# Optimization experiments

Hardware: AMD Instinct MI355X
Metric: run time of the kernel (lower is better)

The kernel has to match this reference:

```python
import jax, jax.numpy as jnp
import numpy as np

N_ADAPTERS = 16
RANK = 16
ALPHA = 16.0
SCALING = ALPHA / RANK
B, S, IN, OUT = 32, 512, 1024, 4096


def setup_inputs() -> dict:
    key = jax.random.key(0)
    k1, k2, k3, k4, k5, k6 = jax.random.split(key, 6)
    hidden_states = jax.random.normal(k1, (B, S, IN), dtype=jnp.float32)
    adapter_ids = jax.random.randint(k2, (B,), 0, N_ADAPTERS, dtype=jnp.int64)
    W = jax.random.normal(k3, (IN, OUT), dtype=jnp.float32) * 0.02
    b = jax.random.normal(k4, (OUT,), dtype=jnp.float32) * 0.02
    lora_a = jax.random.normal(k5, (N_ADAPTERS, IN, RANK), dtype=jnp.float32) * (1.0 / np.sqrt(IN))
    lora_b = jax.random.normal(k6, (N_ADAPTERS, RANK, OUT), dtype=jnp.float32) * 0.02
    return {"hidden_states": hidden_states, "adapter_ids": adapter_ids,
            "W": W, "b": b, "lora_a": lora_a, "lora_b": lora_b}


def reference(hidden_states, adapter_ids, W, b, lora_a, lora_b):
    # Base Conv1D (GPT-2 style): x @ W + b  -> [B, S, OUT]
    base_output = jnp.einsum('bsi,io->bso', hidden_states, W) + b
    # Per-sample adapter gather (replaces the unique-id loop + boolean masks):
    a_sel = lora_a[adapter_ids]          # [B, IN, R]
    b_sel = lora_b[adapter_ids]          # [B, R, OUT]
    low_rank = jnp.einsum('bsi,bir->bsr', hidden_states, a_sel)   # [B, S, R]
    delta = jnp.einsum('bsr,bro->bso', low_rank, b_sel) * SCALING # [B, S, OUT]
    return base_output + delta
```

## Files before the change

kernel.cpp:

```cpp
#include <hip/hip_runtime.h>

#define M_TOT 16384
#define N_TOT 4096
#define K_TOT 1024
#define R_LORA 16

#define BM 256
#define BN 256
#define BK 64
#define NSTEP 64

typedef __attribute__((ext_vector_type(8))) short bf16x8_t;
typedef __attribute__((ext_vector_type(4))) float f32x4_t;

__device__ __forceinline__ unsigned short f2bf(float f) {
  unsigned u = __builtin_bit_cast(unsigned, f);
  u += 0x7FFFu + ((u >> 16) & 1u);
  return (unsigned short)(u >> 16);
}

__device__ __forceinline__ void gload_lds16(const void* g, void* l) {
  __builtin_amdgcn_global_load_lds(
      (const __attribute__((address_space(1))) unsigned int*)g,
      (__attribute__((address_space(3))) unsigned int*)l, 16, 0, 0);
}

__global__ __launch_bounds__(256) void prep_kernel(const float* __restrict__ x,
                                                   const float* __restrict__ W,
                                                   const float* __restrict__ lora_a,
                                                   const float* __restrict__ lora_b,
                                                   unsigned short* __restrict__ xB,
                                                   unsigned short* __restrict__ WtB,
                                                   unsigned short* __restrict__ AtB,
                                                   unsigned short* __restrict__ lbT) {
  __shared__ float lds[64][65];
  const int bid = blockIdx.x;
  const int t = threadIdx.x;
  if (bid < 1024) {
    size_t i = (size_t)bid * 256 + t;
    const size_t stride = (size_t)1024 * 256;
    const size_t n4 = (size_t)M_TOT * K_TOT / 4;
    for (; i < n4; i += stride) {
      float4 v = ((const float4*)x)[i];
      ushort4 h;
      h.x = f2bf(v.x); h.y = f2bf(v.y); h.z = f2bf(v.z); h.w = f2bf(v.w);
      ((ushort4*)xB)[i] = h;
    }
  } else if (bid < 2048) {
    const int v = bid - 1024;
    const int k0 = (v & 15) * 64;
    const int n0 = (v >> 4) * 64;
    const int rr = t >> 4;
    const int cc = (t & 15) * 4;
#pragma unroll
    for (int i = 0; i < 4; ++i) {
      int row = i * 16 + rr;
      float4 w4 = *(const float4*)(W + (size_t)(k0 + row) * N_TOT + n0 + cc);
      lds[row][cc + 0] = w4.x; lds[row][cc + 1] = w4.y;
      lds[row][cc + 2] = w4.z; lds[row][cc + 3] = w4.w;
    }
    __syncthreads();
#pragma unroll
    for (int i = 0; i < 4; ++i) {
      int nrow = i * 16 + rr;
      ushort4 h;
      h.x = f2bf(lds[cc + 0][nrow]); h.y = f2bf(lds[cc + 1][nrow]);
      h.z = f2bf(lds[cc + 2][nrow]); h.w = f2bf(lds[cc + 3][nrow]);
      *(ushort4*)(WtB + (size_t)(n0 + nrow) * K_TOT + k0 + cc) = h;
    }
  } else {
    const int b2 = bid - 2048;
    if (b2 < 64) {
      int idx = b2 * 256 + t;
      int aid = idx >> 10;
      int k = idx & 1023;
      const float* src = lora_a + (size_t)idx * 16;
#pragma unroll
      for (int q = 0; q < 4; ++q) {
        float4 v4 = ((const float4*)src)[q];
#pragma unroll
        for (int j = 0; j < 4; ++j) {
          int r = q * 4 + j;
          float val = (j == 0) ? v4.x : (j == 1) ? v4.y : (j == 2) ? v4.z : v4.w;
          AtB[(((size_t)aid * 16 + r) << 10) + k] = f2bf(val);
        }
      }
    } else {
      int idx = (b2 - 64) * 256 + t;
      int aid = idx >> 12;
      int n = idx & 4095;
      unsigned short o[16];
#pragma unroll
      for (int r = 0; r < 16; ++r)
        o[r] = f2bf(lora_b[((size_t)aid * 16 + r) * N_TOT + n]);
      ushort4* dst = (ushort4*)(lbT + ((size_t)aid * N_TOT + n) * 16);
#pragma unroll
      for (int q = 0; q < 4; ++q) {
        ushort4 h; h.x = o[q*4+0]; h.y = o[q*4+1]; h.z = o[q*4+2]; h.w = o[q*4+3];
        dst[q] = h;
      }
    }
  }
}

__global__ __launch_bounds__(256) void lowrank_kernel(const unsigned short* __restrict__ xB,
                                                      const unsigned short* __restrict__ AtB,
                                                      const int* __restrict__ aids,
                                                      unsigned short* __restrict__ lrB) {
  __shared__ char As[128 * 128];
  const int blk = blockIdx.x;
  const int t = threadIdx.x;
  const int lane = t & 63;
  const int w = t >> 6;
  const int fr = lane & 15, fq = lane >> 4;
  const int aid = aids[blk >> 2];

  const unsigned short* aSrc[4];
  char* aDst[4];
#pragma unroll
  for (int r = 0; r < 4; ++r) {
    int off = (r * 256 + t) * 16;
    int row = off >> 7, cb = off & 127;
    int sb = cb ^ ((row & 7) << 4);
    aSrc[r] = xB + (size_t)(blk * 128 + row) * K_TOT + (sb >> 1);
    aDst[r] = As + off;
  }
  const unsigned short* bBase = AtB + ((size_t)aid * 16 + fr) * K_TOT + fq * 8;

  f32x4_t acc[2];
  acc[0] = (f32x4_t){0.f, 0.f, 0.f, 0.f};
  acc[1] = (f32x4_t){0.f, 0.f, 0.f, 0.f};

  for (int kt = 0; kt < K_TOT / 64; ++kt) {
#pragma unroll
    for (int r = 0; r < 4; ++r) gload_lds16(aSrc[r] + kt * 64, aDst[r]);
    __syncthreads();
#pragma unroll
    for (int ks = 0; ks < 2; ++ks) {
      bf16x8_t bfr = *(const bf16x8_t*)(bBase + kt * 64 + ks * 32);
#pragma unroll
      for (int m = 0; m < 2; ++m) {
        int row = w * 32 + m * 16 + fr;
        int cb = ks * 64 + fq * 16;
        bf16x8_t af = *(const bf16x8_t*)(As + row * 128 + (cb ^ ((row & 7) << 4)));
        acc[m] = __builtin_amdgcn_mfma_f32_16x16x32_bf16(af, bfr, acc[m], 0, 0, 0);
      }
    }
    __syncthreads();
  }
#pragma unroll
  for (int m = 0; m < 2; ++m) {
    int gm0 = blk * 128 + w * 32 + m * 16 + fq * 4;
#pragma unroll
    for (int q = 0; q < 4; ++q)
      lrB[(size_t)(gm0 + q) * R_LORA + fr] = f2bf(acc[m][q]);
  }
}

#define STAGE_HALF(gbase, koff, ldsbase)                                   \
  do {                                                                     \
    gload_lds16((const char*)(gbase) + (koff), (ldsbase) + t * 16);        \
    gload_lds16((const char*)(gbase) + 64 * 2048 + (koff),                 \
                (ldsbase) + 8192 + t * 16);                                \
  } while (0)

#define MM(AS, BS, MH, NH)                                                 \
  do {                                                                     \
    __builtin_amdgcn_s_setprio(1);                                         \
    _Pragma("unroll") for (int ks = 0; ks < 2; ++ks)                       \
      _Pragma("unroll") for (int m = 0; m < 4; ++m)                        \
        _Pragma("unroll") for (int n = 0; n < 2; ++n)                      \
          acc[(MH) * 4 + m][(NH) * 2 + n] =                                \
              __builtin_amdgcn_mfma_f32_16x16x32_bf16(                     \
                  AS[m][ks], BS[n][ks],                                    \
                  acc[(MH) * 4 + m][(NH) * 2 + n], 0, 0, 0);               \
    __builtin_amdgcn_s_setprio(0);                                         \
  } while (0)

__global__ __launch_bounds__(512, 2) void gemm_kernel(
    const unsigned short* __restrict__ xB, const unsigned short* __restrict__ WtB,
    const unsigned short* __restrict__ lrB, const unsigned short* __restrict__ lbT,
    const float* __restrict__ bias, const int* __restrict__ aids,
    float* __restrict__ out) {
  __shared__ char smem[131072];

  const int orig = blockIdx.x;
  const int xcd = orig & 7;
  const int j = orig >> 3;
  const int tn = xcd * 2 + (j & 1);
  const int tmg = j >> 1;

  const int t = threadIdx.x;
  const int lane = t & 63;
  const int wid = t >> 6;
  const int wr = wid >> 2;
  const int wc = wid & 3;
  const int fr = lane & 15, fq = lane >> 4;

  const int laneA = fr * 128 + (((fq << 4) ^ ((fr & 7) << 4)));
  const int waveAoff = wr * 16384;
  const int waveBoff = 32768 + (wc >> 1) * 16384 + (wc & 1) * 8192;

  const int srow = t >> 3;
  const int sb = (((t & 7) ^ (srow & 7)) << 4);
  const char* pAbase = (const char*)xB + (size_t)(tmg * 1024 + srow) * 2048 + sb;
  const char* pBpanel = (const char*)WtB + (size_t)(tn * 256 + srow) * 2048 + sb;

  f32x4_t acc[8][4];
#pragma unroll
  for (int m = 0; m < 8; ++m)
#pragma unroll
    for (int n = 0; n < 4; ++n) acc[m][n] = (f32x4_t){0.f, 0.f, 0.f, 0.f};

  STAGE_HALF(pAbase, 0, smem + 0);
  STAGE_HALF(pAbase + (size_t)128 * 2048, 0, smem + 16384);
  STAGE_HALF(pBpanel, 0, smem + 32768);
  STAGE_HALF(pBpanel + (size_t)128 * 2048, 0, smem + 49152);
  __syncthreads();

#pragma unroll 1
  for (int s = 0; s < NSTEP; ++s) {
    char* base = smem + ((s & 1) << 16);
    char* nbase = smem + (((s + 1) & 1) << 16);
    char* bufA = base + waveAoff;
    char* bufB = base + waveBoff;

    const int u1 = s + 1;
    if (u1 < NSTEP) {
      const char* pA1 = pAbase + (size_t)(u1 >> 4) * (256 * 2048);
      const int k1 = (u1 & 15) * 128;
      STAGE_HALF(pA1, k1, nbase + 0);
      STAGE_HALF(pA1 + (size_t)128 * 2048, k1, nbase + 16384);
      STAGE_HALF(pBpanel, k1, nbase + 32768);
      STAGE_HALF(pBpanel + (size_t)128 * 2048, k1, nbase + 49152);
    }

    bf16x8_t a0F[4][2], a1F[4][2], b0F[2][2], b1F[2][2];
#pragma unroll
    for (int n = 0; n < 2; ++n)
#pragma unroll
      for (int ks = 0; ks < 2; ++ks)
        b0F[n][ks] = *(const bf16x8_t*)(bufB + n * 2048 + (laneA ^ (ks << 6)));
#pragma unroll
    for (int m = 0; m < 4; ++m)
#pragma unroll
      for (int ks = 0; ks < 2; ++ks)
        a0F[m][ks] = *(const bf16x8_t*)(bufA + m * 2048 + (laneA ^ (ks << 6)));
#pragma unroll
    for (int n = 0; n < 2; ++n)
#pragma unroll
      for (int ks = 0; ks < 2; ++ks)
        b1F[n][ks] = *(const bf16x8_t*)(bufB + 4096 + n * 2048 + (laneA ^ (ks << 6)));
#pragma unroll
    for (int m = 0; m < 4; ++m)
#pragma unroll
      for (int ks = 0; ks < 2; ++ks)
        a1F[m][ks] = *(const bf16x8_t*)(bufA + 8192 + m * 2048 + (laneA ^ (ks << 6)));

    MM(a0F, b0F, 0, 0);
    MM(a0F, b1F, 0, 1);
    MM(a1F, b1F, 1, 1);
    MM(a1F, b0F, 1, 0);

    if ((s & 15) == 15) {
      const int tm = tmg * 4 + (s >> 4);
      const int aid = aids[tm >> 1];
      bf16x8_t z8 = (bf16x8_t){0, 0, 0, 0, 0, 0, 0, 0};
      bf16x8_t lrf[8], lbf[4];
#pragma unroll
      for (int m = 0; m < 8; ++m) lrf[m] = z8;
#pragma unroll
      for (int n = 0; n < 4; ++n) lbf[n] = z8;
      if (fq < 2) {
#pragma unroll
        for (int m = 0; m < 8; ++m)
          lrf[m] = *(const bf16x8_t*)(lrB + (size_t)(tm * 256 + wr * 128 + m * 16 + fr) * R_LORA + fq * 8);
#pragma unroll
        for (int n = 0; n < 4; ++n)
          lbf[n] = *(const bf16x8_t*)(lbT + ((size_t)aid * N_TOT + tn * 256 + wc * 64 + n * 16 + fr) * R_LORA + fq * 8);
      }
#pragma unroll
      for (int m = 0; m < 8; ++m)
#pragma unroll
        for (int n = 0; n < 4; ++n)
          acc[m][n] = __builtin_amdgcn_mfma_f32_16x16x32_bf16(lrf[m], lbf[n], acc[m][n], 0, 0, 0);

#pragma unroll
      for (int n = 0; n < 4; ++n) {
        int gn = tn * 256 + wc * 64 + n * 16 + fr;
        float bv = bias[gn];
#pragma unroll
        for (int m = 0; m < 8; ++m) {
          int gm0 = tm * 256 + wr * 128 + m * 16 + fq * 4;
          float* op = out + (size_t)gm0 * N_TOT + gn;
#pragma unroll
          for (int q = 0; q < 4; ++q) op[(size_t)q * N_TOT] = acc[m][n][q] + bv;
        }
      }
#pragma unroll
      for (int m = 0; m < 8; ++m)
#pragma unroll
        for (int n = 0; n < 4; ++n) acc[m][n] = (f32x4_t){0.f, 0.f, 0.f, 0.f};
    }

    __syncthreads();
  }
}

extern "C" void kernel_launch(void* const* d_in, const int* in_sizes, int n_in,
                              void* d_out, int out_size, void* d_ws, size_t ws_size,
                              hipStream_t stream) {
  const float* x      = (const float*)d_in[0];
  const int*   aids   = (const int*)d_in[1];
  const float* W      = (const float*)d_in[2];
  const float* bias   = (const float*)d_in[3];
  const float* lora_a = (const float*)d_in[4];
  const float* lora_b = (const float*)d_in[5];
  float* out = (float*)d_out;

  char* ws = (char*)d_ws;
  unsigned short* xB  = (unsigned short*)(ws);
  unsigned short* WtB = (unsigned short*)(ws + (size_t)32 * 1024 * 1024);
  unsigned short* lrB = (unsigned short*)(ws + (size_t)40 * 1024 * 1024);
  unsigned short* AtB = (unsigned short*)(ws + (size_t)40 * 1024 * 1024 + 512 * 1024);
  unsigned short* lbT = (unsigned short*)(ws + (size_t)41 * 1024 * 1024);

  prep_kernel<<<2368, 256, 0, stream>>>(x, W, lora_a, lora_b, xB, WtB, AtB, lbT);
  lowrank_kernel<<<128, 256, 0, stream>>>(xB, AtB, aids, lrB);
  gemm_kernel<<<256, 512, 0, stream>>>(xB, WtB, lrB, lbT, bias, aids, out);
}
```

Before: 207.6 us.

## Fuse low-rank LoRA projection into prep kernel and unroll GEMM loop by two

The separate lowrank kernel is folded into the prep kernel. Each of 128 blocks now converts its own 128-row slice of x to bf16, transposes the selected adapter's lora_a into LDS, and computes the rank-16 projection right away, which removes one launch and the AtB workspace round trip. The x conversion is now spread over only 128 blocks instead of 1024, so that part of prep may become a longer critical path. The GEMM main loop is also unrolled by two so the double-buffer selector is a compile-time constant and the epilogue check is skipped on even steps.

```diff
diff --git a/kernel.cpp b/kernel.cpp
--- a/kernel.cpp
+++ b/kernel.cpp
@@ -25,29 +25,94 @@
       (__attribute__((address_space(3))) unsigned int*)l, 16, 0, 0);
 }
 
+#define AT_LDE 1032
 __global__ __launch_bounds__(256) void prep_kernel(const float* __restrict__ x,
                                                    const float* __restrict__ W,
                                                    const float* __restrict__ lora_a,
                                                    const float* __restrict__ lora_b,
+                                                   const int* __restrict__ aids,
                                                    unsigned short* __restrict__ xB,
                                                    unsigned short* __restrict__ WtB,
-                                                   unsigned short* __restrict__ AtB,
+                                                   unsigned short* __restrict__ lrB,
                                                    unsigned short* __restrict__ lbT) {
-  __shared__ float lds[64][65];
+  __shared__ char smem_prep[16 * AT_LDE * 2 + 16384];
   const int bid = blockIdx.x;
   const int t = threadIdx.x;
-  if (bid < 1024) {
-    size_t i = (size_t)bid * 256 + t;
-    const size_t stride = (size_t)1024 * 256;
-    const size_t n4 = (size_t)M_TOT * K_TOT / 4;
-    for (; i < n4; i += stride) {
-      float4 v = ((const float4*)x)[i];
+
+  if (bid < 128) {
+    const int blk = bid;
+    const int aid = aids[blk >> 2];
+    unsigned short* At = (unsigned short*)smem_prep;
+    char* As = smem_prep + 16 * AT_LDE * 2;
+
+    const float* Asrc = lora_a + (size_t)aid * (K_TOT * R_LORA);
+    for (int i = t; i < 4096; i += 256) {
+      float4 v = ((const float4*)Asrc)[i];
+      int k = i >> 2;
+      int r0 = (i & 3) * 4;
+      At[(r0 + 0) * AT_LDE + k] = f2bf(v.x);
+      At[(r0 + 1) * AT_LDE + k] = f2bf(v.y);
+      At[(r0 + 2) * AT_LDE + k] = f2bf(v.z);
+      At[(r0 + 3) * AT_LDE + k] = f2bf(v.w);
+    }
+
+    const float* xsrc = x + (size_t)blk * 128 * K_TOT;
+    unsigned short* xdst = xB + (size_t)blk * 128 * K_TOT;
+    for (int i = t; i < 32768; i += 256) {
+      float4 v = ((const float4*)xsrc)[i];
       ushort4 h;
       h.x = f2bf(v.x); h.y = f2bf(v.y); h.z = f2bf(v.z); h.w = f2bf(v.w);
-      ((ushort4*)xB)[i] = h;
-    }
-  } else if (bid < 2048) {
-    const int v = bid - 1024;
+      ((ushort4*)xdst)[i] = h;
+    }
+    __syncthreads();
+
+    const int lane = t & 63;
+    const int w = t >> 6;
+    const int fr = lane & 15, fq = lane >> 4;
+
+    const unsigned short* aSrc[4];
+    char* aDst[4];
+#pragma unroll
+    for (int r = 0; r < 4; ++r) {
+      int off = (r * 256 + t) * 16;
+      int row = off >> 7, cb = off & 127;
+      int sb = cb ^ ((row & 7) << 4);
+      aSrc[r] = xB + (size_t)(blk * 128 + row) * K_TOT + (sb >> 1);
+      aDst[r] = As + off;
+    }
+    const unsigned short* bBase = At + fr * AT_LDE + fq * 8;
+
+    f32x4_t acc[2];
+    acc[0] = (f32x4_t){0.f, 0.f, 0.f, 0.f};
+    acc[1] = (f32x4_t){0.f, 0.f, 0.f, 0.f};
+
+    for (int kt = 0; kt < K_TOT / 64; ++kt) {
+#pragma unroll
+      for (int r = 0; r < 4; ++r) gload_lds16(aSrc[r] + kt * 64, aDst[r]);
+      __syncthreads();
+#pragma unroll
+      for (int ks = 0; ks < 2; ++ks) {
+        bf16x8_t bfr = *(const bf16x8_t*)(bBase + kt * 64 + ks * 32);
+#pragma unroll
+        for (int m = 0; m < 2; ++m) {
+          int row = w * 32 + m * 16 + fr;
+          int cb = ks * 64 + fq * 16;
+          bf16x8_t af = *(const bf16x8_t*)(As + row * 128 + (cb ^ ((row & 7) << 4)));
+          acc[m] = __builtin_amdgcn_mfma_f32_16x16x32_bf16(af, bfr, acc[m], 0, 0, 0);
+        }
+      }
+      __syncthreads();
+    }
+#pragma unroll
+    for (int m = 0; m < 2; ++m) {
+      int gm0 = blk * 128 + w * 32 + m * 16 + fq * 4;
+#pragma unroll
+      for (int q = 0; q < 4; ++q)
+        lrB[(size_t)(gm0 + q) * R_LORA + fr] = f2bf(acc[m][q]);
+    }
+  } else if (bid < 1152) {
+    float (*lds)[65] = (float(*)[65])smem_prep;
+    const int v = bid - 128;
     const int k0 = (v & 15) * 64;
     const int n0 = (v >> 4) * 64;
     const int rr = t >> 4;
@@ -69,91 +134,19 @@
       *(ushort4*)(WtB + (size_t)(n0 + nrow) * K_TOT + k0 + cc) = h;
     }
   } else {
-    const int b2 = bid - 2048;
-    if (b2 < 64) {
-      int idx = b2 * 256 + t;
-      int aid = idx >> 10;
-      int k = idx & 1023;
-      const float* src = lora_a + (size_t)idx * 16;
-#pragma unroll
-      for (int q = 0; q < 4; ++q) {
-        float4 v4 = ((const float4*)src)[q];
-#pragma unroll
-        for (int j = 0; j < 4; ++j) {
-          int r = q * 4 + j;
-          float val = (j == 0) ? v4.x : (j == 1) ? v4.y : (j == 2) ? v4.z : v4.w;
-          AtB[(((size_t)aid * 16 + r) << 10) + k] = f2bf(val);
-        }
-      }
-    } else {
-      int idx = (b2 - 64) * 256 + t;
-      int aid = idx >> 12;
-      int n = idx & 4095;
-      unsigned short o[16];
-#pragma unroll
-      for (int r = 0; r < 16; ++r)
-        o[r] = f2bf(lora_b[((size_t)aid * 16 + r) * N_TOT + n]);
-      ushort4* dst = (ushort4*)(lbT + ((size_t)aid * N_TOT + n) * 16);
-#pragma unroll
-      for (int q = 0; q < 4; ++q) {
-        ushort4 h; h.x = o[q*4+0]; h.y = o[q*4+1]; h.z = o[q*4+2]; h.w = o[q*4+3];
-        dst[q] = h;
-      }
-    }
-  }
-}
-
-__global__ __launch_bounds__(256) void lowrank_kernel(const unsigned short* __restrict__ xB,
-                                                      const unsigned short* __restrict__ AtB,
-                                                      const int* __restrict__ aids,
-                                                      unsigned short* __restrict__ lrB) {
-  __shared__ char As[128 * 128];
-  const int blk = blockIdx.x;
-  const int t = threadIdx.x;
-  const int lane = t & 63;
-  const int w = t >> 6;
-  const int fr = lane & 15, fq = lane >> 4;
-  const int aid = aids[blk >> 2];
-
-  const unsigned short* aSrc[4];
-  char* aDst[4];
-#pragma unroll
-  for (int r = 0; r < 4; ++r) {
-    int off = (r * 256 + t) * 16;
-    int row = off >> 7, cb = off & 127;
-    int sb = cb ^ ((row & 7) << 4);
-    aSrc[r] = xB + (size_t)(blk * 128 + row) * K_TOT + (sb >> 1);
-    aDst[r] = As + off;
-  }
-  const unsigned short* bBase = AtB + ((size_t)aid * 16 + fr) * K_TOT + fq * 8;
-
-  f32x4_t acc[2];
-  acc[0] = (f32x4_t){0.f, 0.f, 0.f, 0.f};
-  acc[1] = (f32x4_t){0.f, 0.f, 0.f, 0.f};
-
-  for (int kt = 0; kt < K_TOT / 64; ++kt) {
-#pragma unroll
-    for (int r = 0; r < 4; ++r) gload_lds16(aSrc[r] + kt * 64, aDst[r]);
-    __syncthreads();
-#pragma unroll
-    for (int ks = 0; ks < 2; ++ks) {
-      bf16x8_t bfr = *(const bf16x8_t*)(bBase + kt * 64 + ks * 32);
-#pragma unroll
-      for (int m = 0; m < 2; ++m) {
-        int row = w * 32 + m * 16 + fr;
-        int cb = ks * 64 + fq * 16;
-        bf16x8_t af = *(const bf16x8_t*)(As + row * 128 + (cb ^ ((row & 7) << 4)));
-        acc[m] = __builtin_amdgcn_mfma_f32_16x16x32_bf16(af, bfr, acc[m], 0, 0, 0);
-      }
-    }
-    __syncthreads();
-  }
-#pragma unroll
-  for (int m = 0; m < 2; ++m) {
-    int gm0 = blk * 128 + w * 32 + m * 16 + fq * 4;
-#pragma unroll
-    for (int q = 0; q < 4; ++q)
-      lrB[(size_t)(gm0 + q) * R_LORA + fr] = f2bf(acc[m][q]);
+    int idx = (bid - 1152) * 256 + t;
+    int aid = idx >> 12;
+    int n = idx & 4095;
+    unsigned short o[16];
+#pragma unroll
+    for (int r = 0; r < 16; ++r)
+      o[r] = f2bf(lora_b[((size_t)aid * 16 + r) * N_TOT + n]);
+    ushort4* dst = (ushort4*)(lbT + ((size_t)aid * N_TOT + n) * 16);
+#pragma unroll
+    for (int q = 0; q < 4; ++q) {
+      ushort4 h; h.x = o[q*4+0]; h.y = o[q*4+1]; h.z = o[q*4+2]; h.w = o[q*4+3];
+      dst[q] = h;
+    }
   }
 }
 
@@ -177,6 +170,72 @@
     __builtin_amdgcn_s_setprio(0);                                         \
   } while (0)
 
+#define KSTEP(S, BUFSEL, EPI)                                              \
+  do {                                                                     \
+    const int s_ = (S);                                                    \
+    char* base = smem + ((BUFSEL) << 16);                                  \
+    char* nbase = smem + (((BUFSEL) ^ 1) << 16);                           \
+    char* bufA = base + waveAoff;                                          \
+    char* bufB = base + waveBoff;                                          \
+    const int u1 = s_ + 1;                                                 \
+    if (u1 < NSTEP) {                                                      \
+      const char* pA1 = pAbase + (size_t)(u1 >> 4) * (256 * 2048);         \
+      const int k1 = (u1 & 15) * 128;                                      \
+      STAGE_HALF(pA1, k1, nbase + 0);                                      \
+      STAGE_HALF(pA1 + (size_t)128 * 2048, k1, nbase + 16384);             \
+      STAGE_HALF(pBpanel, k1, nbase + 32768);                              \
+      STAGE_HALF(pBpanel + (size_t)128 * 2048, k1, nbase + 49152);         \
+    }                                                                      \
+    bf16x8_t a0F[4][2], a1F[4][2], b0F[2][2], b1F[2][2];                   \
+    _Pragma("unroll") for (int n = 0; n < 2; ++n)                          \
+      _Pragma("unroll") for (int ks = 0; ks < 2; ++ks)                     \
+        b0F[n][ks] = *(const bf16x8_t*)(bufB + n * 2048 + (laneA ^ (ks << 6))); \
+    _Pragma("unroll") for (int m = 0; m < 4; ++m)                          \
+      _Pragma("unroll") for (int ks = 0; ks < 2; ++ks)                     \
+        a0F[m][ks] = *(const bf16x8_t*)(bufA + m * 2048 + (laneA ^ (ks << 6))); \
+    _Pragma("unroll") for (int n = 0; n < 2; ++n)                          \
+      _Pragma("unroll") for (int ks = 0; ks < 2; ++ks)                     \
+        b1F[n][ks] = *(const bf16x8_t*)(bufB + 4096 + n * 2048 + (laneA ^ (ks << 6))); \
+    _Pragma("unroll") for (int m = 0; m < 4; ++m)                          \
+      _Pragma("unroll") for (int ks = 0; ks < 2; ++ks)                     \
+        a1F[m][ks] = *(const bf16x8_t*)(bufA + 8192 + m * 2048 + (laneA ^ (ks << 6))); \
+    MM(a0F, b0F, 0, 0);                                                    \
+    MM(a0F, b1F, 0, 1);                                                    \
+    MM(a1F, b1F, 1, 1);                                                    \
+    MM(a1F, b0F, 1, 0);                                                    \
+    if ((EPI) && (s_ & 15) == 15) {                                        \
+      const int tm = tmg * 4 + (s_ >> 4);                                  \
+      const int aid = aids[tm >> 1];                                       \
+      bf16x8_t z8 = (bf16x8_t){0, 0, 0, 0, 0, 0, 0, 0};                    \
+      bf16x8_t lrf[8], lbf[4];                                             \
+      _Pragma("unroll") for (int m = 0; m < 8; ++m) lrf[m] = z8;           \
+      _Pragma("unroll") for (int n = 0; n < 4; ++n) lbf[n] = z8;           \
+      if (fq < 2) {                                                        \
+        _Pragma("unroll") for (int m = 0; m < 8; ++m)                      \
+          lrf[m] = *(const bf16x8_t*)(lrB + (size_t)(tm * 256 + wr * 128 + m * 16 + fr) * R_LORA + fq * 8); \
+        _Pragma("unroll") for (int n = 0; n < 4; ++n)                      \
+          lbf[n] = *(const bf16x8_t*)(lbT + ((size_t)aid * N_TOT + tn * 256 + wc * 64 + n * 16 + fr) * R_LORA + fq * 8); \
+      }                                                                    \
+      _Pragma("unroll") for (int m = 0; m < 8; ++m)                        \
+        _Pragma("unroll") for (int n = 0; n < 4; ++n)                      \
+          acc[m][n] = __builtin_amdgcn_mfma_f32_16x16x32_bf16(lrf[m], lbf[n], acc[m][n], 0, 0, 0); \
+      _Pragma("unroll") for (int n = 0; n < 4; ++n) {                      \
+        int gn = tn * 256 + wc * 64 + n * 16 + fr;                         \
+        float bv = bias[gn];                                               \
+        _Pragma("unroll") for (int m = 0; m < 8; ++m) {                    \
+          int gm0 = tm * 256 + wr * 128 + m * 16 + fq * 4;                 \
+          float* op = out + (size_t)gm0 * N_TOT + gn;                      \
+          _Pragma("unroll") for (int q = 0; q < 4; ++q)                    \
+            op[(size_t)q * N_TOT] = acc[m][n][q] + bv;                     \
+        }                                                                  \
+      }                                                                    \
+      _Pragma("unroll") for (int m = 0; m < 8; ++m)                        \
+        _Pragma("unroll") for (int n = 0; n < 4; ++n)                      \
+          acc[m][n] = (f32x4_t){0.f, 0.f, 0.f, 0.f};                       \
+    }                                                                      \
+    __syncthreads();                                                       \
+  } while (0)
+
 __global__ __launch_bounds__(512, 2) void gemm_kernel(
     const unsigned short* __restrict__ xB, const unsigned short* __restrict__ WtB,
     const unsigned short* __restrict__ lrB, const unsigned short* __restrict__ lbT,
@@ -219,91 +278,9 @@
   __syncthreads();
 
 #pragma unroll 1
-  for (int s = 0; s < NSTEP; ++s) {
-    char* base = smem + ((s & 1) << 16);
-    char* nbase = smem + (((s + 1) & 1) << 16);
-    char* bufA = base + waveAoff;
-    char* bufB = base + waveBoff;
-
-    const int u1 = s + 1;
-    if (u1 < NSTEP) {
-      const char* pA1 = pAbase + (size_t)(u1 >> 4) * (256 * 2048);
-      const int k1 = (u1 & 15) * 128;
-      STAGE_HALF(pA1, k1, nbase + 0);
-      STAGE_HALF(pA1 + (size_t)128 * 2048, k1, nbase + 16384);
-      STAGE_HALF(pBpanel, k1, nbase + 32768);
-      STAGE_HALF(pBpanel + (size_t)128 * 2048, k1, nbase + 49152);
-    }
-
-    bf16x8_t a0F[4][2], a1F[4][2], b0F[2][2], b1F[2][2];
-#pragma unroll
-    for (int n = 0; n < 2; ++n)
-#pragma unroll
-      for (int ks = 0; ks < 2; ++ks)
-        b0F[n][ks] = *(const bf16x8_t*)(bufB + n * 2048 + (laneA ^ (ks << 6)));
-#pragma unroll
-    for (int m = 0; m < 4; ++m)
-#pragma unroll
-      for (int ks = 0; ks < 2; ++ks)
-        a0F[m][ks] = *(const bf16x8_t*)(bufA + m * 2048 + (laneA ^ (ks << 6)));
-#pragma unroll
-    for (int n = 0; n < 2; ++n)
-#pragma unroll
-      for (int ks = 0; ks < 2; ++ks)
-        b1F[n][ks] = *(const bf16x8_t*)(bufB + 4096 + n * 2048 + (laneA ^ (ks << 6)));
-#pragma unroll
-    for (int m = 0; m < 4; ++m)
-#pragma unroll
-      for (int ks = 0; ks < 2; ++ks)
-        a1F[m][ks] = *(const bf16x8_t*)(bufA + 8192 + m * 2048 + (laneA ^ (ks << 6)));
-
-    MM(a0F, b0F, 0, 0);
-    MM(a0F, b1F, 0, 1);
-    MM(a1F, b1F, 1, 1);
-    MM(a1F, b0F, 1, 0);
-
-    if ((s & 15) == 15) {
-      const int tm = tmg * 4 + (s >> 4);
-      const int aid = aids[tm >> 1];
-      bf16x8_t z8 = (bf16x8_t){0, 0, 0, 0, 0, 0, 0, 0};
-      bf16x8_t lrf[8], lbf[4];
-#pragma unroll
-      for (int m = 0; m < 8; ++m) lrf[m] = z8;
-#pragma unroll
-      for (int n = 0; n < 4; ++n) lbf[n] = z8;
-      if (fq < 2) {
-#pragma unroll
-        for (int m = 0; m < 8; ++m)
-          lrf[m] = *(const bf16x8_t*)(lrB + (size_t)(tm * 256 + wr * 128 + m * 16 + fr) * R_LORA + fq * 8);
-#pragma unroll
-        for (int n = 0; n < 4; ++n)
-          lbf[n] = *(const bf16x8_t*)(lbT + ((size_t)aid * N_TOT + tn * 256 + wc * 64 + n * 16 + fr) * R_LORA + fq * 8);
-      }
-#pragma unroll
-      for (int m = 0; m < 8; ++m)
-#pragma unroll
-        for (int n = 0; n < 4; ++n)
-          acc[m][n] = __builtin_amdgcn_mfma_f32_16x16x32_bf16(lrf[m], lbf[n], acc[m][n], 0, 0, 0);
-
-#pragma unroll
-      for (int n = 0; n < 4; ++n) {
-        int gn = tn * 256 + wc * 64 + n * 16 + fr;
-        float bv = bias[gn];
-#pragma unroll
-        for (int m = 0; m < 8; ++m) {
-          int gm0 = tm * 256 + wr * 128 + m * 16 + fq * 4;
-          float* op = out + (size_t)gm0 * N_TOT + gn;
-#pragma unroll
-          for (int q = 0; q < 4; ++q) op[(size_t)q * N_TOT] = acc[m][n][q] + bv;
-        }
-      }
-#pragma unroll
-      for (int m = 0; m < 8; ++m)
-#pragma unroll
-        for (int n = 0; n < 4; ++n) acc[m][n] = (f32x4_t){0.f, 0.f, 0.f, 0.f};
-    }
-
-    __syncthreads();
+  for (int s2 = 0; s2 < NSTEP; s2 += 2) {
+    KSTEP(s2, 0, 0);
+    KSTEP(s2 + 1, 1, 1);
   }
 }
 
@@ -322,10 +299,8 @@
   unsigned short* xB  = (unsigned short*)(ws);
   unsigned short* WtB = (unsigned short*)(ws + (size_t)32 * 1024 * 1024);
   unsigned short* lrB = (unsigned short*)(ws + (size_t)40 * 1024 * 1024);
-  unsigned short* AtB = (unsigned short*)(ws + (size_t)40 * 1024 * 1024 + 512 * 1024);
   unsigned short* lbT = (unsigned short*)(ws + (size_t)41 * 1024 * 1024);
 
-  prep_kernel<<<2368, 256, 0, stream>>>(x, W, lora_a, lora_b, xB, WtB, AtB, lbT);
-  lowrank_kernel<<<128, 256, 0, stream>>>(xB, AtB, aids, lrB);
+  prep_kernel<<<1408, 256, 0, stream>>>(x, W, lora_a, lora_b, aids, xB, WtB, lrB, lbT);
   gemm_kernel<<<256, 512, 0, stream>>>(xB, WtB, lrB, lbT, bias, aids, out);
 }
```

Result: slower. 281.5 us (+35.6%).

## Split GEMM into two half-N kernels with finer-grained pipelined staging variant

Applied to the files above, without the earlier changes.

Replaces the persistent 256-block GEMM, which walked four M tiles per block, with one-tile-per-block kernels over 512 workgroups. The N range is split in half: gemm_v1 keeps the original double-buffered schedule for the first eight N tiles, and gemm_v2 handles the last eight. gemm_v2 interleaves partial LDS fragment loads, staged global-to-LDS copies (B prefetched two tiles ahead) and MFMA quarters, separated by explicit barriers and waitcnt, to overlap memory with compute. This adds an extra kernel launch and hand-tuned vmcnt/lgkmcnt counts, which could race if they are miscounted.

```diff
diff --git a/kernel.cpp b/kernel.cpp
--- a/kernel.cpp
+++ b/kernel.cpp
@@ -4,11 +4,7 @@
 #define N_TOT 4096
 #define K_TOT 1024
 #define R_LORA 16
-
-#define BM 256
-#define BN 256
-#define BK 64
-#define NSTEP 64
+#define NTILES 16
 
 typedef __attribute__((ext_vector_type(8))) short bf16x8_t;
 typedef __attribute__((ext_vector_type(4))) float f32x4_t;
@@ -131,7 +127,7 @@
   acc[0] = (f32x4_t){0.f, 0.f, 0.f, 0.f};
   acc[1] = (f32x4_t){0.f, 0.f, 0.f, 0.f};
 
-  for (int kt = 0; kt < K_TOT / 64; ++kt) {
+  for (int kt = 0; kt < 16; ++kt) {
 #pragma unroll
     for (int r = 0; r < 4; ++r) gload_lds16(aSrc[r] + kt * 64, aDst[r]);
     __syncthreads();
@@ -157,6 +153,9 @@
   }
 }
 
+#define BAR() __builtin_amdgcn_s_barrier()
+#define WAIT_LGKM0() asm volatile("s_waitcnt lgkmcnt(0)" ::: "memory")
+
 #define STAGE_HALF(gbase, koff, ldsbase)                                   \
   do {                                                                     \
     gload_lds16((const char*)(gbase) + (koff), (ldsbase) + t * 16);        \
@@ -164,7 +163,7 @@
                 (ldsbase) + 8192 + t * 16);                                \
   } while (0)
 
-#define MM(AS, BS, MH, NH)                                                 \
+#define MMQ(AS, BS, MH, NH)                                                \
   do {                                                                     \
     __builtin_amdgcn_s_setprio(1);                                         \
     _Pragma("unroll") for (int ks = 0; ks < 2; ++ks)                       \
@@ -177,64 +176,84 @@
     __builtin_amdgcn_s_setprio(0);                                         \
   } while (0)
 
-__global__ __launch_bounds__(512, 2) void gemm_kernel(
+#define GEMM_PREAMBLE()                                                    \
+  const int t = threadIdx.x;                                               \
+  const int lane = t & 63;                                                 \
+  const int wid = t >> 6;                                                  \
+  const int wr = wid >> 2;                                                 \
+  const int wc = wid & 3;                                                  \
+  const int fr = lane & 15, fq = lane >> 4;                                \
+  const int laneA = fr * 128 + (((fq << 4) ^ ((fr & 7) << 4)));            \
+  const int waveAoff = wr * 16384;                                         \
+  const int waveBoff = 32768 + (wc >> 1) * 16384 + (wc & 1) * 8192;        \
+  const int srow = t >> 3;                                                 \
+  const int sb = (((t & 7) ^ (srow & 7)) << 4);                            \
+  const char* pA = (const char*)xB + (size_t)(tm * 256 + srow) * 2048 + sb;\
+  const char* pB = (const char*)WtB + (size_t)(tn * 256 + srow) * 2048 + sb;\
+  f32x4_t acc[8][4];                                                       \
+  _Pragma("unroll") for (int m = 0; m < 8; ++m)                            \
+    _Pragma("unroll") for (int n = 0; n < 4; ++n)                          \
+      acc[m][n] = (f32x4_t){0.f, 0.f, 0.f, 0.f};
+
+#define GEMM_EPILOGUE()                                                    \
+  do {                                                                     \
+    const int aid = aids[tm >> 1];                                         \
+    bf16x8_t z8 = (bf16x8_t){0, 0, 0, 0, 0, 0, 0, 0};                      \
+    bf16x8_t lrf[8], lbf[4];                                               \
+    _Pragma("unroll") for (int m = 0; m < 8; ++m) lrf[m] = z8;             \
+    _Pragma("unroll") for (int n = 0; n < 4; ++n) lbf[n] = z8;             \
+    if (fq < 2) {                                                          \
+      _Pragma("unroll") for (int m = 0; m < 8; ++m)                        \
+        lrf[m] = *(const bf16x8_t*)(lrB + (size_t)(tm * 256 + wr * 128 + m * 16 + fr) * R_LORA + fq * 8); \
+      _Pragma("unroll") for (int n = 0; n < 4; ++n)                        \
+        lbf[n] = *(const bf16x8_t*)(lbT + ((size_t)aid * N_TOT + tn * 256 + wc * 64 + n * 16 + fr) * R_LORA + fq * 8); \
+    }                                                                      \
+    _Pragma("unroll") for (int m = 0; m < 8; ++m)                          \
+      _Pragma("unroll") for (int n = 0; n < 4; ++n)                        \
+        acc[m][n] = __builtin_amdgcn_mfma_f32_16x16x32_bf16(lrf[m], lbf[n], acc[m][n], 0, 0, 0); \
+    _Pragma("unroll") for (int n = 0; n < 4; ++n) {                        \
+      int gn = tn * 256 + wc * 64 + n * 16 + fr;                           \
+      float bv = bias[gn];                                                 \
+      _Pragma("unroll") for (int m = 0; m < 8; ++m) {                      \
+        int gm0 = tm * 256 + wr * 128 + m * 16 + fq * 4;                   \
+        float* op = out + (size_t)gm0 * N_TOT + gn;                        \
+        _Pragma("unroll") for (int q = 0; q < 4; ++q)                      \
+          op[(size_t)q * N_TOT] = acc[m][n][q] + bv;                       \
+      }                                                                    \
+    }                                                                      \
+  } while (0)
+
+__global__ __launch_bounds__(512, 2) void gemm_v1(
     const unsigned short* __restrict__ xB, const unsigned short* __restrict__ WtB,
     const unsigned short* __restrict__ lrB, const unsigned short* __restrict__ lbT,
     const float* __restrict__ bias, const int* __restrict__ aids,
     float* __restrict__ out) {
   __shared__ char smem[131072];
-
   const int orig = blockIdx.x;
-  const int xcd = orig & 7;
-  const int j = orig >> 3;
-  const int tn = xcd * 2 + (j & 1);
-  const int tmg = j >> 1;
-
-  const int t = threadIdx.x;
-  const int lane = t & 63;
-  const int wid = t >> 6;
-  const int wr = wid >> 2;
-  const int wc = wid & 3;
-  const int fr = lane & 15, fq = lane >> 4;
-
-  const int laneA = fr * 128 + (((fq << 4) ^ ((fr & 7) << 4)));
-  const int waveAoff = wr * 16384;
-  const int waveBoff = 32768 + (wc >> 1) * 16384 + (wc & 1) * 8192;
-
-  const int srow = t >> 3;
-  const int sb = (((t & 7) ^ (srow & 7)) << 4);
-  const char* pAbase = (const char*)xB + (size_t)(tmg * 1024 + srow) * 2048 + sb;
-  const char* pBpanel = (const char*)WtB + (size_t)(tn * 256 + srow) * 2048 + sb;
-
-  f32x4_t acc[8][4];
-#pragma unroll
-  for (int m = 0; m < 8; ++m)
-#pragma unroll
-    for (int n = 0; n < 4; ++n) acc[m][n] = (f32x4_t){0.f, 0.f, 0.f, 0.f};
-
-  STAGE_HALF(pAbase, 0, smem + 0);
-  STAGE_HALF(pAbase + (size_t)128 * 2048, 0, smem + 16384);
-  STAGE_HALF(pBpanel, 0, smem + 32768);
-  STAGE_HALF(pBpanel + (size_t)128 * 2048, 0, smem + 49152);
+  const int wg = (orig & 7) * 64 + (orig >> 3);
+  const int tn = wg & 7;
+  const int tm = wg >> 3;
+  GEMM_PREAMBLE();
+
+  STAGE_HALF(pA, 0, smem + 0);
+  STAGE_HALF(pA + (size_t)128 * 2048, 0, smem + 16384);
+  STAGE_HALF(pB, 0, smem + 32768);
+  STAGE_HALF(pB + (size_t)128 * 2048, 0, smem + 49152);
   __syncthreads();
 
 #pragma unroll 1
-  for (int s = 0; s < NSTEP; ++s) {
+  for (int s = 0; s < NTILES; ++s) {
     char* base = smem + ((s & 1) << 16);
     char* nbase = smem + (((s + 1) & 1) << 16);
     char* bufA = base + waveAoff;
     char* bufB = base + waveBoff;
-
-    const int u1 = s + 1;
-    if (u1 < NSTEP) {
-      const char* pA1 = pAbase + (size_t)(u1 >> 4) * (256 * 2048);
-      const int k1 = (u1 & 15) * 128;
-      STAGE_HALF(pA1, k1, nbase + 0);
-      STAGE_HALF(pA1 + (size_t)128 * 2048, k1, nbase + 16384);
-      STAGE_HALF(pBpanel, k1, nbase + 32768);
-      STAGE_HALF(pBpanel + (size_t)128 * 2048, k1, nbase + 49152);
-    }
-
+    if (s + 1 < NTILES) {
+      const int k1 = (s + 1) * 128;
+      STAGE_HALF(pA, k1, nbase + 0);
+      STAGE_HALF(pA + (size_t)128 * 2048, k1, nbase + 16384);
+      STAGE_HALF(pB, k1, nbase + 32768);
+      STAGE_HALF(pB + (size_t)128 * 2048, k1, nbase + 49152);
+    }
     bf16x8_t a0F[4][2], a1F[4][2], b0F[2][2], b1F[2][2];
 #pragma unroll
     for (int n = 0; n < 2; ++n)
@@ -256,55 +275,97 @@
 #pragma unroll
       for (int ks = 0; ks < 2; ++ks)
         a1F[m][ks] = *(const bf16x8_t*)(bufA + 8192 + m * 2048 + (laneA ^ (ks << 6)));
-
-    MM(a0F, b0F, 0, 0);
-    MM(a0F, b1F, 0, 1);
-    MM(a1F, b1F, 1, 1);
-    MM(a1F, b0F, 1, 0);
-
-    if ((s & 15) == 15) {
-      const int tm = tmg * 4 + (s >> 4);
-      const int aid = aids[tm >> 1];
-      bf16x8_t z8 = (bf16x8_t){0, 0, 0, 0, 0, 0, 0, 0};
-      bf16x8_t lrf[8], lbf[4];
-#pragma unroll
-      for (int m = 0; m < 8; ++m) lrf[m] = z8;
-#pragma unroll
-      for (int n = 0; n < 4; ++n) lbf[n] = z8;
-      if (fq < 2) {
-#pragma unroll
-        for (int m = 0; m < 8; ++m)
-          lrf[m] = *(const bf16x8_t*)(lrB + (size_t)(tm * 256 + wr * 128 + m * 16 + fr) * R_LORA + fq * 8);
-#pragma unroll
-        for (int n = 0; n < 4; ++n)
-          lbf[n] = *(const bf16x8_t*)(lbT + ((size_t)aid * N_TOT + tn * 256 + wc * 64 + n * 16 + fr) * R_LORA + fq * 8);
-      }
-#pragma unroll
-      for (int m = 0; m < 8; ++m)
-#pragma unroll
-        for (int n = 0; n < 4; ++n)
-          acc[m][n] = __builtin_amdgcn_mfma_f32_16x16x32_bf16(lrf[m], lbf[n], acc[m][n], 0, 0, 0);
-
-#pragma unroll
-      for (int n = 0; n < 4; ++n) {
-        int gn = tn * 256 + wc * 64 + n * 16 + fr;
-        float bv = bias[gn];
-#pragma unroll
-        for (int m = 0; m < 8; ++m) {
-          int gm0 = tm * 256 + wr * 128 + m * 16 + fq * 4;
-          float* op = out + (size_t)gm0 * N_TOT + gn;
-#pragma unroll
-          for (int q = 0; q < 4; ++q) op[(size_t)q * N_TOT] = acc[m][n][q] + bv;
-        }
-      }
-#pragma unroll
-      for (int m = 0; m < 8; ++m)
-#pragma unroll
-        for (int n = 0; n < 4; ++n) acc[m][n] = (f32x4_t){0.f, 0.f, 0.f, 0.f};
-    }
-
+    MMQ(a0F, b0F, 0, 0);
+    MMQ(a0F, b1F, 0, 1);
+    MMQ(a1F, b1F, 1, 1);
+    MMQ(a1F, b0F, 1, 0);
     __syncthreads();
   }
+  GEMM_EPILOGUE();
+}
+
+#define LDA2(buf, MH)                                                      \
+  do {                                                                     \
+    _Pragma("unroll") for (int m = 0; m < 4; ++m)                          \
+      _Pragma("unroll") for (int ks = 0; ks < 2; ++ks)                     \
+        aF[m][ks] = *(const bf16x8_t*)((buf) + waveAoff + (MH) * 8192 +    \
+                                       m * 2048 + (laneA ^ (ks << 6)));    \
+  } while (0)
+
+#define LDB2(buf, dst, NH)                                                 \
+  do {                                                                     \
+    _Pragma("unroll") for (int n = 0; n < 2; ++n)                          \
+      _Pragma("unroll") for (int ks = 0; ks < 2; ++ks)                     \
+        dst[n][ks] = *(const bf16x8_t*)((buf) + waveBoff + (NH) * 4096 +   \
+                                        n * 2048 + (laneA ^ (ks << 6)));   \
+  } while (0)
+
+#define TILE4(T, cb, ob, VMN)                                              \
+  do {                                                                     \
+                                                                   \
+    LDA2(cb, 0);                                                           \
+    LDB2(cb, bF0, 0);                                                      \
+    if ((T) + 1 < NTILES) STAGE_HALF(pA, ((T) + 1) * 128, (ob) + 0);       \
+    asm volatile("s_waitcnt lgkmcnt(8)" ::: "memory");                     \
+    BAR(); WAIT_LGKM0();                                                   \
+    MMQ(aF, bF0, 0, 0);                                                    \
+    BAR();                                                                 \
+                                                                   \
+    LDB2(cb, bF1, 1);                                                      \
+    if ((T) + 1 < NTILES)                                                  \
+      STAGE_HALF(pA + (size_t)128 * 2048, ((T) + 1) * 128, (ob) + 16384);  \
+    BAR(); WAIT_LGKM0();                                                   \
+    MMQ(aF, bF1, 0, 1);                                                    \
+    BAR();                                                                 \
+                                                                   \
+    LDA2(cb, 1);                                                           \
+    if ((T) + 2 < NTILES) STAGE_HALF(pB, ((T) + 2) * 128, (cb) + 32768);   \
+    BAR(); WAIT_LGKM0();                                                   \
+    MMQ(aF, bF1, 1, 1);                                                    \
+    BAR();                                                                 \
+                                                                   \
+    if ((T) + 2 < NTILES)                                                  \
+      STAGE_HALF(pB + (size_t)128 * 2048, ((T) + 2) * 128, (cb) + 49152);  \
+    BAR();                                                                 \
+    MMQ(aF, bF0, 1, 0);                                                    \
+    if ((VMN) == 6) asm volatile("s_waitcnt vmcnt(6)" ::: "memory");       \
+    else if ((VMN) == 2) asm volatile("s_waitcnt vmcnt(2)" ::: "memory");  \
+    BAR();                                                                 \
+  } while (0)
+
+__global__ __launch_bounds__(512, 2) void gemm_v2(
+    const unsigned short* __restrict__ xB, const unsigned short* __restrict__ WtB,
+    const unsigned short* __restrict__ lrB, const unsigned short* __restrict__ lbT,
+    const float* __restrict__ bias, const int* __restrict__ aids,
+    float* __restrict__ out) {
+  __shared__ char smem[131072];
+  const int orig = blockIdx.x;
+  const int wg = (orig & 7) * 64 + (orig >> 3);
+  const int tn = 8 + (wg & 7);
+  const int tm = wg >> 3;
+  GEMM_PREAMBLE();
+  char* const b0 = smem;
+  char* const b1 = smem + 65536;
+
+  bf16x8_t aF[4][2];
+  bf16x8_t bF0[2][2], bF1[2][2];
+
+  STAGE_HALF(pA, 0, b0 + 0);
+  STAGE_HALF(pA + (size_t)128 * 2048, 0, b0 + 16384);
+  STAGE_HALF(pB, 0, b0 + 32768);
+  STAGE_HALF(pB + (size_t)128 * 2048, 0, b0 + 49152);
+  STAGE_HALF(pB, 128, b1 + 32768);
+  STAGE_HALF(pB + (size_t)128 * 2048, 128, b1 + 49152);
+  asm volatile("s_waitcnt vmcnt(4)" ::: "memory");
+  BAR();
+
+#pragma unroll 1
+  for (int i = 0; i < NTILES / 2; ++i) {
+    const int T = 2 * i;
+    TILE4(T, b0, b1, (T <= 12 ? 6 : 2));
+    TILE4(T + 1, b1, b0, (T + 1 <= 13 ? 6 : 9));
+  }
+  GEMM_EPILOGUE();
 }
 
 extern "C" void kernel_launch(void* const* d_in, const int* in_sizes, int n_in,
@@ -327,5 +388,6 @@
 
   prep_kernel<<<2368, 256, 0, stream>>>(x, W, lora_a, lora_b, xB, WtB, AtB, lbT);
   lowrank_kernel<<<128, 256, 0, stream>>>(xB, AtB, aids, lrB);
-  gemm_kernel<<<256, 512, 0, stream>>>(xB, WtB, lrB, lbT, bias, aids, out);
-}
+  gemm_v1<<<512, 512, 0, stream>>>(xB, WtB, lrB, lbT, bias, aids, out);
+  gemm_v2<<<512, 512, 0, stream>>>(xB, WtB, lrB, lbT, bias, aids, out);
+}
```

Measured after the change: 231.2 us. +11.4%, slower.

## Fuse low-rank LoRA projection into prep kernel, dropping separate lowrank launch

Applied to the files above, without the earlier changes.

Removes the separate lowrank kernel and the lora_a transpose pass. 512 extra blocks in the prep kernel now read fp32 x directly, convert it to bf16 in LDS, and compute x·A with scalar FMAs into a per-thread rank-16 accumulator, then reduce across threads through LDS. This saves one kernel launch and the reread of xB. In exchange it re-reads fp32 x, uses scalar FMAs instead of MFMA, and raises prep LDS use to 48KB, which may lower occupancy for the conversion blocks.

```diff
diff --git a/kernel.cpp b/kernel.cpp
--- a/kernel.cpp
+++ b/kernel.cpp
@@ -4,10 +4,6 @@
 #define N_TOT 4096
 #define K_TOT 1024
 #define R_LORA 16
-
-#define BM 256
-#define BN 256
-#define BK 64
 #define NSTEP 64
 
 typedef __attribute__((ext_vector_type(8))) short bf16x8_t;
@@ -18,6 +14,9 @@
   u += 0x7FFFu + ((u >> 16) & 1u);
   return (unsigned short)(u >> 16);
 }
+__device__ __forceinline__ float bf2f(unsigned short u) {
+  return __builtin_bit_cast(float, (unsigned)u << 16);
+}
 
 __device__ __forceinline__ void gload_lds16(const void* g, void* l) {
   __builtin_amdgcn_global_load_lds(
@@ -29,13 +28,15 @@
                                                    const float* __restrict__ W,
                                                    const float* __restrict__ lora_a,
                                                    const float* __restrict__ lora_b,
+                                                   const int* __restrict__ aids,
                                                    unsigned short* __restrict__ xB,
                                                    unsigned short* __restrict__ WtB,
-                                                   unsigned short* __restrict__ AtB,
+                                                   unsigned short* __restrict__ lrB,
                                                    unsigned short* __restrict__ lbT) {
-  __shared__ float lds[64][65];
+  __shared__ char prep_smem[49152];
   const int bid = blockIdx.x;
   const int t = threadIdx.x;
+
   if (bid < 1024) {
     size_t i = (size_t)bid * 256 + t;
     const size_t stride = (size_t)1024 * 256;
@@ -47,6 +48,7 @@
       ((ushort4*)xB)[i] = h;
     }
   } else if (bid < 2048) {
+    float (*lds)[65] = (float(*)[65])prep_smem;
     const int v = bid - 1024;
     const int k0 = (v & 15) * 64;
     const int n0 = (v >> 4) * 64;
@@ -68,92 +70,84 @@
       h.z = f2bf(lds[cc + 2][nrow]); h.w = f2bf(lds[cc + 3][nrow]);
       *(ushort4*)(WtB + (size_t)(n0 + nrow) * K_TOT + k0 + cc) = h;
     }
+  } else if (bid < 2304) {
+    int idx = (bid - 2048) * 256 + t;
+    int aid = idx >> 12;
+    int n = idx & 4095;
+    unsigned short o[16];
+#pragma unroll
+    for (int r = 0; r < 16; ++r)
+      o[r] = f2bf(lora_b[((size_t)aid * 16 + r) * N_TOT + n]);
+    ushort4* dst = (ushort4*)(lbT + ((size_t)aid * N_TOT + n) * 16);
+#pragma unroll
+    for (int q = 0; q < 4; ++q) {
+      ushort4 h; h.x = o[q*4+0]; h.y = o[q*4+1]; h.z = o[q*4+2]; h.w = o[q*4+3];
+      dst[q] = h;
+    }
   } else {
-    const int b2 = bid - 2048;
-    if (b2 < 64) {
-      int idx = b2 * 256 + t;
-      int aid = idx >> 10;
-      int k = idx & 1023;
-      const float* src = lora_a + (size_t)idx * 16;
-#pragma unroll
-      for (int q = 0; q < 4; ++q) {
-        float4 v4 = ((const float4*)src)[q];
-#pragma unroll
-        for (int j = 0; j < 4; ++j) {
-          int r = q * 4 + j;
-          float val = (j == 0) ? v4.x : (j == 1) ? v4.y : (j == 2) ? v4.z : v4.w;
-          AtB[(((size_t)aid * 16 + r) << 10) + k] = f2bf(val);
-        }
+    const int blk = bid - 2304;
+    const int row0 = blk * 32;
+    const int aid = aids[blk >> 4];
+    unsigned short* A_lds = (unsigned short*)prep_smem;
+    unsigned short* x_lds = (unsigned short*)(prep_smem + 32768);
+    float* red = (float*)(prep_smem + 32768);
+
+    const float* Asrc = lora_a + (size_t)aid * (K_TOT * R_LORA);
+#pragma unroll
+    for (int it = 0; it < 16; ++it) {
+      int i = it * 256 + t;
+      float4 v = ((const float4*)Asrc)[i];
+      int k = i >> 2;
+      int r0 = (i & 3) * 4;
+      A_lds[(r0 + 0) * 1024 + k] = f2bf(v.x);
+      A_lds[(r0 + 1) * 1024 + k] = f2bf(v.y);
+      A_lds[(r0 + 2) * 1024 + k] = f2bf(v.z);
+      A_lds[(r0 + 3) * 1024 + k] = f2bf(v.w);
+    }
+
+    float acc[16];
+#pragma unroll
+    for (int r = 0; r < 16; ++r) acc[r] = 0.f;
+
+    const int rr = t & 31;
+    const int wq = t >> 5;
+
+#pragma unroll 1
+    for (int c = 0; c < 8; ++c) {
+#pragma unroll
+      for (int it = 0; it < 4; ++it) {
+        int idx = it * 256 + t;
+        int row = idx >> 5;
+        int col = (idx & 31) * 4;
+        float4 v = *(const float4*)(x + (size_t)(row0 + row) * K_TOT + c * 128 + col);
+        ushort4 h;
+        h.x = f2bf(v.x); h.y = f2bf(v.y); h.z = f2bf(v.z); h.w = f2bf(v.w);
+        *(ushort4*)(x_lds + row * 132 + col) = h;
       }
-    } else {
-      int idx = (b2 - 64) * 256 + t;
-      int aid = idx >> 12;
-      int n = idx & 4095;
-      unsigned short o[16];
-#pragma unroll
-      for (int r = 0; r < 16; ++r)
-        o[r] = f2bf(lora_b[((size_t)aid * 16 + r) * N_TOT + n]);
-      ushort4* dst = (ushort4*)(lbT + ((size_t)aid * N_TOT + n) * 16);
-#pragma unroll
-      for (int q = 0; q < 4; ++q) {
-        ushort4 h; h.x = o[q*4+0]; h.y = o[q*4+1]; h.z = o[q*4+2]; h.w = o[q*4+3];
-        dst[q] = h;
+      __syncthreads();
+#pragma unroll
+      for (int kk = 0; kk < 16; ++kk) {
+        int kc = wq * 16 + kk;
+        float xv = bf2f(x_lds[rr * 132 + kc]);
+#pragma unroll
+        for (int r = 0; r < 16; ++r)
+          acc[r] += xv * bf2f(A_lds[r * 1024 + c * 128 + kc]);
       }
-    }
-  }
-}
-
-__global__ __launch_bounds__(256) void lowrank_kernel(const unsigned short* __restrict__ xB,
-                                                      const unsigned short* __restrict__ AtB,
-                                                      const int* __restrict__ aids,
-                                                      unsigned short* __restrict__ lrB) {
-  __shared__ char As[128 * 128];
-  const int blk = blockIdx.x;
-  const int t = threadIdx.x;
-  const int lane = t & 63;
-  const int w = t >> 6;
-  const int fr = lane & 15, fq = lane >> 4;
-  const int aid = aids[blk >> 2];
-
-  const unsigned short* aSrc[4];
-  char* aDst[4];
-#pragma unroll
-  for (int r = 0; r < 4; ++r) {
-    int off = (r * 256 + t) * 16;
-    int row = off >> 7, cb = off & 127;
-    int sb = cb ^ ((row & 7) << 4);
-    aSrc[r] = xB + (size_t)(blk * 128 + row) * K_TOT + (sb >> 1);
-    aDst[r] = As + off;
-  }
-  const unsigned short* bBase = AtB + ((size_t)aid * 16 + fr) * K_TOT + fq * 8;
-
-  f32x4_t acc[2];
-  acc[0] = (f32x4_t){0.f, 0.f, 0.f, 0.f};
-  acc[1] = (f32x4_t){0.f, 0.f, 0.f, 0.f};
-
-  for (int kt = 0; kt < K_TOT / 64; ++kt) {
-#pragma unroll
-    for (int r = 0; r < 4; ++r) gload_lds16(aSrc[r] + kt * 64, aDst[r]);
+      __syncthreads();
+    }
+
+#pragma unroll
+    for (int r = 0; r < 16; ++r) red[t * 16 + r] = acc[r];
     __syncthreads();
 #pragma unroll
-    for (int ks = 0; ks < 2; ++ks) {
-      bf16x8_t bfr = *(const bf16x8_t*)(bBase + kt * 64 + ks * 32);
-#pragma unroll
-      for (int m = 0; m < 2; ++m) {
-        int row = w * 32 + m * 16 + fr;
-        int cb = ks * 64 + fq * 16;
-        bf16x8_t af = *(const bf16x8_t*)(As + row * 128 + (cb ^ ((row & 7) << 4)));
-        acc[m] = __builtin_amdgcn_mfma_f32_16x16x32_bf16(af, bfr, acc[m], 0, 0, 0);
-      }
-    }
-    __syncthreads();
-  }
-#pragma unroll
-  for (int m = 0; m < 2; ++m) {
-    int gm0 = blk * 128 + w * 32 + m * 16 + fq * 4;
-#pragma unroll
-    for (int q = 0; q < 4; ++q)
-      lrB[(size_t)(gm0 + q) * R_LORA + fr] = f2bf(acc[m][q]);
+    for (int h = 0; h < 2; ++h) {
+      int o = h * 256 + t;
+      int row = o >> 4, r = o & 15;
+      float s = 0.f;
+#pragma unroll
+      for (int q = 0; q < 8; ++q) s += red[(q * 32 + row) * 16 + r];
+      lrB[(size_t)(row0 + row) * R_LORA + r] = f2bf(s);
+    }
   }
 }
 
@@ -322,10 +316,8 @@
   unsigned short* xB  = (unsigned short*)(ws);
   unsigned short* WtB = (unsigned short*)(ws + (size_t)32 * 1024 * 1024);
   unsigned short* lrB = (unsigned short*)(ws + (size_t)40 * 1024 * 1024);
-  unsigned short* AtB = (unsigned short*)(ws + (size_t)40 * 1024 * 1024 + 512 * 1024);
   unsigned short* lbT = (unsigned short*)(ws + (size_t)41 * 1024 * 1024);
 
-  prep_kernel<<<2368, 256, 0, stream>>>(x, W, lora_a, lora_b, xB, WtB, AtB, lbT);
-  lowrank_kernel<<<128, 256, 0, stream>>>(xB, AtB, aids, lrB);
+  prep_kernel<<<2816, 256, 0, stream>>>(x, W, lora_a, lora_b, aids, xB, WtB, lrB, lbT);
   gemm_kernel<<<256, 512, 0, stream>>>(xB, WtB, lrB, lbT, bias, aids, out);
 }
```

Measured after the change: 243.2 us. 17.1% more time.
